# Kernel tuning notes

Measured on AMD Instinct MI355X. Metric: run time of the kernel, lower is better.

The kernel has to match this reference:

```python
import jax, jax.numpy as jnp
import numpy as np

B, S, V, E, H, DM = 4, 512, 32000, 512, 1024, 256
U, M = 4096, 1024
MEM_CAP = 512 * 4  # max_length * memory_segments


def setup_inputs() -> dict:
    key = jax.random.key(0)
    ks = jax.random.split(key, 26)
    def n(k, shape, s=0.02):
        return jax.random.normal(k, shape, dtype=jnp.float32) * s
    return {
        'input_ids': jax.random.randint(ks[0], (B, S), 0, V),
        'past_tokens': jax.random.randint(ks[1], (B, M), 0, V),
        'past_keys': jax.random.normal(ks[2], (B, M, DM), dtype=jnp.float32),
        'untied_ids': jax.random.randint(ks[3], (U,), 0, V),
        'emb': n(ks[4], (V, E)),
        'gru_w_ih': n(ks[5], (3 * H, E)), 'gru_w_hh': n(ks[6], (3 * H, H)),
        'gru_b_ih': n(ks[7], (3 * H,)), 'gru_b_hh': n(ks[8], (3 * H,)),
        'q_w': n(ks[9], (DM, H)), 'q_b': n(ks[10], (DM,)),
        'k_w': n(ks[11], (DM, H)), 'k_b': n(ks[12], (DM,)),
        'gate_w': n(ks[13], (1, H)), 'gate_b': n(ks[14], (1,)),
        'fc_w': n(ks[15], (4 * E, H)), 'fc_b': n(ks[16], (4 * E,)),
        'proj_w': n(ks[17], (E, 4 * E)), 'proj_b': n(ks[18], (E,)),
        'out_bias': jnp.zeros((V,), jnp.float32),
        'part_w': n(ks[19], (U, E)), 'part_b': n(ks[20], (U,)),
        'mem_scale': jnp.float32(6.0),
    }


def _gru(x, w_ih, w_hh, b_ih, b_hh):
    # x: [B,S,E] -> states [B,S,H]; torch GRU cell math
    xp = x @ w_ih.T + b_ih  # [B,S,3H]
    h0 = jnp.zeros((x.shape[0], w_hh.shape[1]), x.dtype)
    def step(h, xp_t):
        hp = h @ w_hh.T + b_hh
        xr, xz, xn = jnp.split(xp_t, 3, axis=-1)
        hr, hz, hn = jnp.split(hp, 3, axis=-1)
        r = jax.nn.sigmoid(xr + hr)
        z = jax.nn.sigmoid(xz + hz)
        nn_ = jnp.tanh(xn + r * hn)
        h_new = (1.0 - z) * nn_ + z * h
        return h_new, h_new
    h_last, states = jax.lax.scan(step, h0, jnp.swapaxes(xp, 0, 1))
    return jnp.swapaxes(states, 0, 1), h_last


def reference(input_ids, past_tokens, past_keys, untied_ids, emb,
              gru_w_ih, gru_w_hh, gru_b_ih, gru_b_hh,
              q_w, q_b, k_w, k_b, gate_w, gate_b,
              fc_w, fc_b, proj_w, proj_b, out_bias, part_w, part_b, mem_scale):
    x = emb[input_ids]                                  # [B,S,E]
    states, _ = _gru(x, gru_w_ih, gru_w_hh, gru_b_ih, gru_b_hh)  # dropout=eval identity
    head = jnp.square(jax.nn.relu(states @ fc_w.T + fc_b))       # [B,S,4E]
    base = head @ proj_w.T + proj_b                                # [B,S,E]
    logits = base @ emb.T + out_bias                               # [B,S,V]
    partial = base @ part_w.T + part_b                             # [B,S,U]
    logits = logits.at[:, :, untied_ids].add(partial)              # scatter_add over vocab

    q = states @ q_w.T + q_b                                       # [B,S,DM]
    ck = states @ k_w.T + k_b                                      # [B,S,DM]
    scale = jnp.float32(1.0 / np.sqrt(DM))
    cur_scores = jnp.einsum('bsd,btd->bst', q, ck) * scale
    causal = jnp.tril(jnp.ones((S, S), bool), k=-1)                # strictly-past mask
    neg = jnp.finfo(cur_scores.dtype).min
    masked_cur = jnp.where(causal[None], cur_scores, neg)
    past_scores = jnp.einsum('bsd,bmd->bsm', q, past_keys) * scale
    all_scores = jnp.concatenate([past_scores, masked_cur], axis=-1)   # [B,S,M+S]
    all_mask = jnp.concatenate([
        jnp.ones((B, S, M), bool),
        jnp.broadcast_to(causal[None], (B, S, S))], axis=-1)
    att = jax.nn.softmax(all_scores, axis=-1) * all_mask
    att = att / jnp.maximum(att.sum(axis=-1, keepdims=True), 1e-6)
    val_idx = jnp.concatenate([
        jnp.broadcast_to(past_tokens[:, None, :], (B, S, M)),
        jnp.broadcast_to(input_ids[:, None, :], (B, S, S))], axis=-1)   # [B,S,M+S]
    gate = jax.nn.sigmoid(states @ gate_w.T + gate_b)               # [B,S,1]
    gated = att * (gate * mem_scale)
    b_idx = jnp.arange(B)[:, None, None]
    s_idx = jnp.arange(S)[None, :, None]
    logits = logits.at[b_idx, s_idx, val_idx].add(gated)            # irregular scatter_add

    next_keys = jax.lax.stop_gradient(
        jnp.concatenate([past_keys, ck], axis=1))[:, -MEM_CAP:]
    next_tokens = jnp.concatenate([past_tokens, input_ids], axis=1)[:, -MEM_CAP:]
    return logits, next_keys, next_tokens
```

## Files before the change

kernel.cpp:

```cpp
#include <hip/hip_runtime.h>
#include <cstddef>
#include <cstring>

#define BB 4
#define SS 512
#define VV 32000
#define EE 512
#define HH 1024
#define DM 256
#define UU 4096
#define MM 1024
#define TT 1536

typedef __attribute__((ext_vector_type(8))) short short8v;
typedef __attribute__((ext_vector_type(4))) float f32x4;

__device__ __forceinline__ unsigned long long agent_ld64(const unsigned long long* p) {
  return __hip_atomic_load(const_cast<unsigned long long*>(p), __ATOMIC_RELAXED,
                           __HIP_MEMORY_SCOPE_AGENT);
}
__device__ __forceinline__ void agent_st64(unsigned long long* p, unsigned long long v) {
  __hip_atomic_store(p, v, __ATOMIC_RELAXED, __HIP_MEMORY_SCOPE_AGENT);
}
__device__ __forceinline__ float sigmoidf_(float x) { return 1.f / (1.f + __expf(-x)); }

__device__ __forceinline__ unsigned short f2bf_rtn(float x) {
  unsigned u; __builtin_memcpy(&u, &x, 4);
  unsigned r = (u + 0x7FFFu + ((u >> 16) & 1u)) >> 16;
  return (unsigned short)r;
}
__device__ __forceinline__ float bf2f(unsigned short b) {
  unsigned u = ((unsigned)b) << 16; float f; __builtin_memcpy(&f, &u, 4); return f;
}

__global__ __launch_bounds__(256) void split_cat(
    const float* __restrict__ in, unsigned short* __restrict__ out, int n, int K)
{
  for (int i = blockIdx.x * 256 + threadIdx.x; i < n; i += gridDim.x * 256) {
    int row = i / K, col = i - row * K;
    float x = in[i];
    unsigned short h = f2bf_rtn(x);
    unsigned short l = f2bf_rtn(x - bf2f(h));
    size_t b = (size_t)row * (K << 1) + col;
    out[b] = h;
    out[b + K] = l;
  }
}

__global__ __launch_bounds__(256) void gemm_mfma_cat(
    const unsigned short* __restrict__ A2, const int* __restrict__ a_idx,
    const unsigned short* __restrict__ W2, const float* __restrict__ bias,
    float* __restrict__ C, unsigned short* __restrict__ C2,
    int K2, int N, int ldc, int act, const int* __restrict__ sidx)
{
  const int tid = threadIdx.x, lane = tid & 63, w = tid >> 6;
  const int bm = blockIdx.y * 128, bn = blockIdx.x * 128;
  const int wm = (w >> 1) * 64, wn = (w & 1) * 64;
  const int r = lane & 15, ko = (lane >> 4) * 8;

  int arow[4];
#pragma unroll
  for (int mi = 0; mi < 4; ++mi) {
    int row = bm + wm + mi * 16 + r;
    arow[mi] = a_idx ? a_idx[row] : row;
  }

  f32x4 acc[4][4] = {};

  for (int k0 = 0; k0 < K2; k0 += 32) {
    short8v a[4], b[4];
#pragma unroll
    for (int mi = 0; mi < 4; ++mi)
      a[mi] = *(const short8v*)(A2 + (size_t)arow[mi] * K2 + k0 + ko);
#pragma unroll
    for (int ni = 0; ni < 4; ++ni)
      b[ni] = *(const short8v*)(W2 + (size_t)(bn + wn + ni * 16 + r) * K2 + k0 + ko);
#pragma unroll
    for (int mi = 0; mi < 4; ++mi)
#pragma unroll
      for (int ni = 0; ni < 4; ++ni)
        acc[mi][ni] = __builtin_amdgcn_mfma_f32_16x16x32_bf16(a[mi], b[ni], acc[mi][ni], 0, 0, 0);
  }

#pragma unroll
  for (int mi = 0; mi < 4; ++mi)
#pragma unroll
    for (int ni = 0; ni < 4; ++ni) {
      const int row = bm + wm + mi * 16 + (lane >> 4) * 4;
      const int col = bn + wn + ni * 16 + (lane & 15);
      const float bv = bias[col];
#pragma unroll
      for (int i = 0; i < 4; ++i) {
        float v = acc[mi][ni][i] + bv;
        if (act == 1) { v = fmaxf(v, 0.f); v *= v; }
        if (C2) {
          unsigned short h = f2bf_rtn(v);
          unsigned short l = f2bf_rtn(v - bf2f(h));
          size_t bo = (size_t)(row + i) * (N << 1) + col;
          C2[bo] = h;
          C2[bo + N] = l;
        } else if (sidx) {
          atomicAdd(C + (size_t)(row + i) * ldc + sidx[col], v);
        } else {
          C[(size_t)(row + i) * ldc + col] = v;
        }
      }
    }
}

__global__ __launch_bounds__(256) void score_mfma_cat(
    const unsigned short* __restrict__ q2,
    const unsigned short* __restrict__ k2,
    float* __restrict__ scores)
{
  const int b = blockIdx.z;
  const unsigned short* A2 = q2 + (size_t)b * SS * (2 * DM);
  const unsigned short* W2 = k2 + (size_t)b * TT * (2 * DM);
  float* C = scores + (size_t)b * SS * TT;

  const int tid = threadIdx.x, lane = tid & 63, w = tid >> 6;
  const int bm = blockIdx.y * 128, bn = blockIdx.x * 128;
  const int wm = (w >> 1) * 64, wn = (w & 1) * 64;
  const int r = lane & 15, ko = (lane >> 4) * 8;

  f32x4 acc[4][4] = {};

  for (int k0 = 0; k0 < 2 * DM; k0 += 32) {
    short8v a[4], bfr[4];
#pragma unroll
    for (int mi = 0; mi < 4; ++mi)
      a[mi] = *(const short8v*)(A2 + (size_t)(bm + wm + mi * 16 + r) * (2 * DM) + k0 + ko);
#pragma unroll
    for (int ni = 0; ni < 4; ++ni)
      bfr[ni] = *(const short8v*)(W2 + (size_t)(bn + wn + ni * 16 + r) * (2 * DM) + k0 + ko);
#pragma unroll
    for (int mi = 0; mi < 4; ++mi)
#pragma unroll
      for (int ni = 0; ni < 4; ++ni)
        acc[mi][ni] = __builtin_amdgcn_mfma_f32_16x16x32_bf16(a[mi], bfr[ni], acc[mi][ni], 0, 0, 0);
  }

#pragma unroll
  for (int mi = 0; mi < 4; ++mi)
#pragma unroll
    for (int ni = 0; ni < 4; ++ni) {
      const int row = bm + wm + mi * 16 + (lane >> 4) * 4;
      const int col = bn + wn + ni * 16 + (lane & 15);
#pragma unroll
      for (int i = 0; i < 4; ++i)
        C[(size_t)(row + i) * TT + col] = acc[mi][ni][i];
    }
}

__global__ __launch_bounds__(256) void softmax_scatter(
    const float* __restrict__ scores,
    const float* __restrict__ ntokf,
    const float* __restrict__ gate,
    const float* __restrict__ msp,
    float* __restrict__ logits)
{
  const int lane = threadIdx.x & 63;
  const int row = (blockIdx.x << 2) + (threadIdx.x >> 6);
  const int b = row >> 9, sg = row & 511;
  const int limit = MM + sg;
  const float* sr = scores + (size_t)row * TT;

  float v[24];
  float mx = -1e30f;
#pragma unroll
  for (int i = 0; i < 24; ++i) {
    int t = (i << 6) + lane;
    v[i] = (t < limit) ? sr[t] * 0.0625f : -1e30f;
    mx = fmaxf(mx, v[i]);
  }
#pragma unroll
  for (int off = 32; off >= 1; off >>= 1) mx = fmaxf(mx, __shfl_xor(mx, off, 64));

  float sum = 0.f;
#pragma unroll
  for (int i = 0; i < 24; ++i) sum += __expf(v[i] - mx);
#pragma unroll
  for (int off = 32; off >= 1; off >>= 1) sum += __shfl_xor(sum, off, 64);

  const float fs = gate[row] * msp[0] / sum;
  const float* tokr = ntokf + b * TT;
  float* lrow = logits + (size_t)row * VV;
#pragma unroll
  for (int i = 0; i < 24; ++i) {
    int t = (i << 6) + lane;
    if (t < limit)
      atomicAdd(lrow + (int)tokr[t], __expf(v[i] - mx) * fs);
  }
}

template <int TILE, int MICRO>
__global__ __launch_bounds__(256) void gemm_k(
    const float* __restrict__ A, const int* __restrict__ a_idx,
    const float* __restrict__ W, const float* __restrict__ bias,
    float* __restrict__ C, int K, int ldc, int act, const int* __restrict__ sidx)
{
  constexpr int PITCH = TILE + 4;
  __shared__ float As[16][PITCH];
  __shared__ float Ws[16][PITCH];
  const int tid = threadIdx.x;
  const int bm = blockIdx.y * TILE, bn = blockIdx.x * TILE;
  const int tr = tid >> 4, tc = tid & 15;
  const int lk = tid & 15, lr0 = tid >> 4;
  float acc[MICRO][MICRO] = {};

  for (int k0 = 0; k0 < K; k0 += 16) {
#pragma unroll
    for (int jj = 0; jj < TILE / 16; ++jj) {
      int row = lr0 + (jj << 4);
      int am = bm + row;
      int ar = a_idx ? a_idx[am] : am;
      As[lk][row] = A[(size_t)ar * K + k0 + lk];
      Ws[lk][row] = W[(size_t)(bn + row) * K + k0 + lk];
    }
    __syncthreads();
#pragma unroll
    for (int kk = 0; kk < 16; ++kk) {
      float av[MICRO], wv[MICRO];
#pragma unroll
      for (int i = 0; i < MICRO; ++i) av[i] = As[kk][tr * MICRO + i];
#pragma unroll
      for (int j = 0; j < MICRO; ++j) wv[j] = Ws[kk][tc * MICRO + j];
#pragma unroll
      for (int i = 0; i < MICRO; ++i)
#pragma unroll
        for (int j = 0; j < MICRO; ++j) acc[i][j] += av[i] * wv[j];
    }
    __syncthreads();
  }

#pragma unroll
  for (int i = 0; i < MICRO; ++i) {
    int m = bm + tr * MICRO + i;
    float tmp[MICRO];
#pragma unroll
    for (int j = 0; j < MICRO; ++j) {
      int n = bn + tc * MICRO + j;
      float v = acc[i][j] + bias[n];
      if (act == 1) { v = fmaxf(v, 0.f); v *= v; }
      tmp[j] = v;
    }
    if (sidx) {
#pragma unroll
      for (int j = 0; j < MICRO; ++j)
        atomicAdd(C + (size_t)m * ldc + sidx[bn + tc * MICRO + j], tmp[j]);
    } else {
      float* cp = C + (size_t)m * ldc + bn + tc * MICRO;
#pragma unroll
      for (int j4 = 0; j4 < MICRO / 4; ++j4)
        *(float4*)(cp + 4 * j4) =
            make_float4(tmp[4 * j4], tmp[4 * j4 + 1], tmp[4 * j4 + 2], tmp[4 * j4 + 3]);
    }
  }
}

__global__ __launch_bounds__(512, 1) void gru_scan(
    const float* __restrict__ xp,
    const float* __restrict__ w_hh,
    const float* __restrict__ b_hh,
    float* __restrict__ states,
    unsigned long long* hbuf)
{
  __shared__ float h_lds[2][HH];
  const int tid = threadIdx.x;
  const int lane = tid & 63;
  const int wv = tid >> 6;
  const int bb = blockIdx.x >> 5;
  const int r = blockIdx.x & 31;
  const int c0 = (r << 5) + (wv << 2);

  unsigned long long* hb = hbuf + ((size_t)bb << 11);

  float wreg[4][3][16];
#pragma unroll
  for (int k = 0; k < 4; ++k)
#pragma unroll
    for (int g = 0; g < 3; ++g) {
      const float* wr = w_hh + (size_t)((g << 10) + c0 + k) * HH + lane;
#pragma unroll
      for (int i = 0; i < 16; ++i) wreg[k][g][i] = wr[i << 6];
    }
  float bh[4][3];
#pragma unroll
  for (int k = 0; k < 4; ++k)
#pragma unroll
    for (int g = 0; g < 3; ++g) bh[k][g] = b_hh[(g << 10) + c0 + k];

  for (int i = tid; i < HH; i += 512) h_lds[0][i] = 0.f;
  __syncthreads();

  for (int t = 0; t < SS; ++t) {
    const int cur = t & 1, nxt = (t + 1) & 1;
    const float* hc = h_lds[cur];

    float4 xrv, xzv, xnv, hold;
    if (lane == 0) {
      const float* xpr = xp + (size_t)((bb << 9) + t) * 3072 + c0;
      xrv = *(const float4*)(xpr);
      xzv = *(const float4*)(xpr + HH);
      xnv = *(const float4*)(xpr + 2 * HH);
      hold = *(const float4*)(hc + c0);
    }

    float acc[4][3] = {};
#pragma unroll
    for (int i = 0; i < 16; ++i) {
      float hv = hc[(i << 6) + lane];
#pragma unroll
      for (int k = 0; k < 4; ++k) {
        acc[k][0] += hv * wreg[k][0][i];
        acc[k][1] += hv * wreg[k][1][i];
        acc[k][2] += hv * wreg[k][2][i];
      }
    }
#pragma unroll
    for (int off = 32; off >= 1; off >>= 1)
#pragma unroll
      for (int k = 0; k < 4; ++k) {
        acc[k][0] += __shfl_xor(acc[k][0], off, 64);
        acc[k][1] += __shfl_xor(acc[k][1], off, 64);
        acc[k][2] += __shfl_xor(acc[k][2], off, 64);
      }

    if (lane == 0) {
      const unsigned long long tagw = ((unsigned long long)(unsigned)(t + 1)) << 32;
      float xr[4] = {xrv.x, xrv.y, xrv.z, xrv.w};
      float xz[4] = {xzv.x, xzv.y, xzv.z, xzv.w};
      float xn[4] = {xnv.x, xnv.y, xnv.z, xnv.w};
      float ho[4] = {hold.x, hold.y, hold.z, hold.w};
      float hv4[4];
#pragma unroll
      for (int k = 0; k < 4; ++k) {
        float rr = sigmoidf_(xr[k] + acc[k][0] + bh[k][0]);
        float zz = sigmoidf_(xz[k] + acc[k][1] + bh[k][1]);
        float nn = tanhf(xn[k] + rr * (acc[k][2] + bh[k][2]));
        hv4[k] = (1.f - zz) * nn + zz * ho[k];
      }
      if (t < SS - 1) {
        unsigned long long* dst = hb + ((size_t)nxt << 10) + c0;
#pragma unroll
        for (int k = 0; k < 4; ++k) {
          unsigned hbits;
          __builtin_memcpy(&hbits, &hv4[k], 4);
          agent_st64(dst + k, tagw | (unsigned long long)hbits);
        }
      }
      *(float4*)(states + (size_t)((bb << 9) + t) * HH + c0) =
          make_float4(hv4[0], hv4[1], hv4[2], hv4[3]);
    }
    if (t == SS - 1) break;

    {
      const unsigned tgt = (unsigned)(t + 1);
      const unsigned long long* src = hb + ((size_t)nxt << 10) + (tid << 1);
      unsigned long long p0, p1;
      for (;;) {
        p0 = agent_ld64(src);
        p1 = agent_ld64(src + 1);
        if ((unsigned)(p0 >> 32) >= tgt && (unsigned)(p1 >> 32) >= tgt) break;
      }
      h_lds[nxt][(tid << 1)] = __uint_as_float((unsigned)p0);
      h_lds[nxt][(tid << 1) + 1] = __uint_as_float((unsigned)p1);
    }
    __syncthreads();
  }
}

__global__ __launch_bounds__(256) void gate_kernel(
    const float* __restrict__ states, const float* __restrict__ gate_w,
    const float* __restrict__ gate_b, float* __restrict__ out)
{
  const int lane = threadIdx.x & 63;
  const int row = (blockIdx.x << 2) + (threadIdx.x >> 6);
  float s = 0.f;
#pragma unroll
  for (int i = 0; i < 16; ++i)
    s += states[(size_t)row * HH + (i << 6) + lane] * gate_w[(i << 6) + lane];
#pragma unroll
  for (int off = 32; off >= 1; off >>= 1) s += __shfl_xor(s, off, 64);
  if (lane == 0) out[row] = sigmoidf_(s + gate_b[0]);
}

__global__ __launch_bounds__(256) void copy_next(
    const float* __restrict__ past_keys, const float* __restrict__ ck,
    const int* __restrict__ past_tokens, const int* __restrict__ input_ids,
    float* __restrict__ nk, float* __restrict__ ntokf)
{
  const int i = blockIdx.x * 256 + threadIdx.x;
  if (i < BB * TT * 64) {
    int b = i / (TT * 64);
    int rem = i - b * (TT * 64);
    int t = rem >> 6, c = rem & 63;
    float4 v;
    if (t < MM) v = ((const float4*)past_keys)[((b << 10) + t) * 64 + c];
    else        v = ((const float4*)ck)[((b << 9) + (t - MM)) * 64 + c];
    ((float4*)nk)[i] = v;
  }
  if (i < BB * TT) {
    int b = i / TT, t = i - b * TT;
    int tok = (t < MM) ? past_tokens[(b << 10) + t] : input_ids[(b << 9) + t - MM];
    ntokf[i] = (float)tok;
  }
}

__global__ __launch_bounds__(256) void attn_scatter(
    const float* __restrict__ qbuf, const float* __restrict__ nk,
    const float* __restrict__ ntokf, const float* __restrict__ gate,
    const float* __restrict__ msp, float* __restrict__ logits)
{
  __shared__ float q_s[8][260];
  __shared__ float k_s[32][260];
  const int b = blockIdx.y;
  const int s0 = blockIdx.x << 3;
  const int tid = threadIdx.x, lane = tid & 63, wv = tid >> 6;
  const int half = lane >> 5, tl = lane & 31;
  const int ss = wv + (half << 2);
  const int sg = s0 + ss;
  const int limit = MM + sg;

  for (int i = tid; i < 8 * 256; i += 256)
    q_s[i >> 8][i & 255] = qbuf[(size_t)((b << 9) + s0 + (i >> 8)) * DM + (i & 255)];

  const int kr = tid >> 3, kc = (tid & 7) << 5;
  float mx = -1e30f, sum = 0.f;
  float fscale = 0.f;

  for (int pass = 0; pass < 2; ++pass) {
    if (pass == 1) {
#pragma unroll
      for (int off = 16; off >= 1; off >>= 1) {
        float mo = __shfl_xor(mx, off, 64);
        float so = __shfl_xor(sum, off, 64);
        float m2 = fmaxf(mx, mo);
        sum = sum * __expf(mx - m2) + so * __expf(mo - m2);
        mx = m2;
      }
      fscale = gate[(b << 9) + sg] * msp[0] / sum;
    }
    for (int tile = 0; tile < 48; ++tile) {
      __syncthreads();
      {
        const float4* src = (const float4*)(nk + ((size_t)(b * TT + (tile << 5) + kr) << 8) + kc);
        float4* dst = (float4*)(&k_s[kr][kc]);
#pragma unroll
        for (int u = 0; u < 8; ++u) dst[u] = src[u];
      }
      __syncthreads();
      int t = (tile << 5) + tl;
      if (t < limit) {
        float a = 0.f;
#pragma unroll 8
        for (int d = 0; d < 256; d += 4) {
          float4 kv = *(const float4*)&k_s[tl][d];
          float4 qv = *(const float4*)&q_s[ss][d];
          a += kv.x * qv.x + kv.y * qv.y + kv.z * qv.z + kv.w * qv.w;
        }
        a *= 0.0625f;
        if (pass == 0) {
          float m2 = fmaxf(mx, a);
          sum = sum * __expf(mx - m2) + __expf(a - m2);
          mx = m2;
        } else {
          int tok = (int)ntokf[b * TT + t];
          atomicAdd(logits + (size_t)((b << 9) + sg) * VV + tok,
                    __expf(a - mx) * fscale);
        }
      }
    }
  }
}

extern "C" void kernel_launch(void* const* d_in, const int* in_sizes, int n_in,
                              void* d_out, int out_size, void* d_ws, size_t ws_size,
                              hipStream_t stream) {
  (void)in_sizes; (void)n_in; (void)out_size;
  const int*   input_ids   = (const int*)  d_in[0];
  const int*   past_tokens = (const int*)  d_in[1];
  const float* past_keys   = (const float*)d_in[2];
  const int*   untied_ids  = (const int*)  d_in[3];
  const float* emb         = (const float*)d_in[4];
  const float* w_ih        = (const float*)d_in[5];
  const float* w_hh        = (const float*)d_in[6];
  const float* b_ih        = (const float*)d_in[7];
  const float* b_hh        = (const float*)d_in[8];
  const float* q_w         = (const float*)d_in[9];
  const float* q_b         = (const float*)d_in[10];
  const float* k_w         = (const float*)d_in[11];
  const float* k_b         = (const float*)d_in[12];
  const float* gate_w      = (const float*)d_in[13];
  const float* gate_b      = (const float*)d_in[14];
  const float* fc_w        = (const float*)d_in[15];
  const float* fc_b        = (const float*)d_in[16];
  const float* proj_w      = (const float*)d_in[17];
  const float* proj_b      = (const float*)d_in[18];
  const float* out_bias    = (const float*)d_in[19];
  const float* part_w      = (const float*)d_in[20];
  const float* part_b      = (const float*)d_in[21];
  const float* mem_scale   = (const float*)d_in[22];

  char* ws = (char*)d_ws;
  float* logits = (float*)d_out;
  float* nk     = logits + 65536000ll;
  float* ntokf  = logits + 67108864ll;

  const bool fast = ws_size >= 180961280ull;

  hipMemsetAsync(ws, 0, 69632, stream);

  if (fast) {
    unsigned long long* hbuf = (unsigned long long*)(ws + 4096);
    float* gatebuf = (float*)(ws + 69632);
    float* xp      = (float*)(ws + 81920);
    float* states  = (float*)(ws + 25247744);
    float* ckb     = (float*)(ws + 33636352);
    unsigned short* emb2    = (unsigned short*)(ws + 35733504);
    unsigned short* w_ih2   = (unsigned short*)(ws + 101269504);
    unsigned short* fc_w2   = (unsigned short*)(ws + 107560960);
    unsigned short* proj_w2 = (unsigned short*)(ws + 115949568);
    unsigned short* part_w2 = (unsigned short*)(ws + 120143872);
    unsigned short* q_w2    = (unsigned short*)(ws + 128532480);
    unsigned short* k_w2    = (unsigned short*)(ws + 129581056);
    unsigned short* states2 = (unsigned short*)(ws + 130629632);
    unsigned short* head2   = (unsigned short*)(ws + 139018240);
    unsigned short* base2   = (unsigned short*)(ws + 155795456);
    unsigned short* qb2     = (unsigned short*)(ws + 159989760);
    unsigned short* nk2     = (unsigned short*)(ws + 162086912);
    float* scores           = (float*)(ws + 168378368);

    split_cat<<<2048, 256, 0, stream>>>(emb, emb2, VV * EE, EE);
    split_cat<<<512, 256, 0, stream>>>(w_ih, w_ih2, 3072 * EE, EE);
    split_cat<<<512, 256, 0, stream>>>(fc_w, fc_w2, 2048 * HH, HH);
    split_cat<<<512, 256, 0, stream>>>(proj_w, proj_w2, EE * 2048, 2048);
    split_cat<<<512, 256, 0, stream>>>(part_w, part_w2, UU * EE, EE);
    split_cat<<<128, 256, 0, stream>>>(q_w, q_w2, DM * HH, HH);
    split_cat<<<128, 256, 0, stream>>>(k_w, k_w2, DM * HH, HH);

    gemm_mfma_cat<<<dim3(3072 / 128, 2048 / 128), 256, 0, stream>>>(
        emb2, input_ids, w_ih2, b_ih, xp, nullptr, 2 * EE, 3072, 3072, 0, nullptr);

    gru_scan<<<128, 512, 0, stream>>>(xp, w_hh, b_hh, states, hbuf);
    split_cat<<<512, 256, 0, stream>>>(states, states2, 2048 * HH, HH);

    gemm_mfma_cat<<<dim3(2048 / 128, 2048 / 128), 256, 0, stream>>>(
        states2, nullptr, fc_w2, fc_b, nullptr, head2, 2 * HH, 2048, 0, 1, nullptr);

    gemm_mfma_cat<<<dim3(512 / 128, 2048 / 128), 256, 0, stream>>>(
        head2, nullptr, proj_w2, proj_b, nullptr, base2, 2 * 2048, EE, 0, 0, nullptr);

    gemm_mfma_cat<<<dim3(VV / 128, 2048 / 128), 256, 0, stream>>>(
        base2, nullptr, emb2, out_bias, logits, nullptr, 2 * EE, VV, VV, 0, nullptr);

    gemm_mfma_cat<<<dim3(UU / 128, 2048 / 128), 256, 0, stream>>>(
        base2, nullptr, part_w2, part_b, logits, nullptr, 2 * EE, UU, VV, 0, untied_ids);

    gemm_mfma_cat<<<dim3(DM / 128, 2048 / 128), 256, 0, stream>>>(
        states2, nullptr, q_w2, q_b, nullptr, qb2, 2 * HH, DM, 0, 0, nullptr);
    gemm_mfma_cat<<<dim3(DM / 128, 2048 / 128), 256, 0, stream>>>(
        states2, nullptr, k_w2, k_b, ckb, nullptr, 2 * HH, DM, DM, 0, nullptr);

    gate_kernel<<<512, 256, 0, stream>>>(states, gate_w, gate_b, gatebuf);

    copy_next<<<1536, 256, 0, stream>>>(past_keys, ckb, past_tokens, input_ids, nk, ntokf);

    split_cat<<<512, 256, 0, stream>>>(nk, nk2, BB * TT * DM, DM);
    score_mfma_cat<<<dim3(TT / 128, SS / 128, BB), 256, 0, stream>>>(qb2, nk2, scores);
    softmax_scatter<<<512, 256, 0, stream>>>(scores, ntokf, gatebuf, mem_scale, logits);
  } else {
    unsigned long long* hbuf = (unsigned long long*)(ws + 4096);
    float* gatebuf  = (float*)(ws + 69632);
    float* qb       = (float*)(ws + 81920);
    float* ckb      = (float*)(ws + 2179072);
    float* xp       = (float*)(ws + 4276224);
    float* states   = (float*)(ws + 29442048);
    float* head     = (float*)(ws + 37830656);
    float* base     = (float*)(ws + 54607872);

    gemm_k<128, 8><<<dim3(3072 / 128, 2048 / 128), 256, 0, stream>>>(
        emb, input_ids, w_ih, b_ih, xp, EE, 3072, 0, nullptr);
    gru_scan<<<128, 512, 0, stream>>>(xp, w_hh, b_hh, states, hbuf);
    gemm_k<128, 8><<<dim3(2048 / 128, 2048 / 128), 256, 0, stream>>>(
        states, nullptr, fc_w, fc_b, head, HH, 2048, 1, nullptr);
    gemm_k<64, 4><<<dim3(512 / 64, 2048 / 64), 256, 0, stream>>>(
        head, nullptr, proj_w, proj_b, base, 2048, EE, 0, nullptr);
    gemm_k<128, 8><<<dim3(VV / 128, 2048 / 128), 256, 0, stream>>>(
        base, nullptr, emb, out_bias, logits, EE, VV, 0, nullptr);
    gemm_k<128, 8><<<dim3(UU / 128, 2048 / 128), 256, 0, stream>>>(
        base, nullptr, part_w, part_b, logits, EE, VV, 0, untied_ids);
    gemm_k<64, 4><<<dim3(DM / 64, 2048 / 64), 256, 0, stream>>>(
        states, nullptr, q_w, q_b, qb, HH, DM, 0, nullptr);
    gemm_k<64, 4><<<dim3(DM / 64, 2048 / 64), 256, 0, stream>>>(
        states, nullptr, k_w, k_b, ckb, HH, DM, 0, nullptr);
    gate_kernel<<<512, 256, 0, stream>>>(states, gate_w, gate_b, gatebuf);
    copy_next<<<1536, 256, 0, stream>>>(past_keys, ckb, past_tokens, input_ids, nk, ntokf);
    attn_scatter<<<dim3(SS / 8, BB), 256, 0, stream>>>(qb, nk, ntokf, gatebuf, mem_scale, logits);
  }
}
```

Before: 4.937 ms.

## Overlap weight bf16 splitting with GRU scan using extra idle blocks

The GRU scan kernel is launched with 64 extra blocks that perform the hi/lo bf16 splitting of the emb, fc, proj, part, q and k weights while the 128 scan blocks run the serial recurrence. The input projection now gathers and splits only the 2048 embedding rows it needs instead of waiting on the full vocabulary split. This moves the split work onto CUs left idle during the latency-bound scan. The risk is that the extra blocks compete for memory bandwidth and could slow the scan's cross-block synchronisation. If the scan relies on all its blocks being co-resident, the larger grid also has to fit on the device at once. The workspace requirement grows to hold the gathered rows.

New measurement: 4.998 ms. Within noise of the previous version (+1.2%).

```diff
diff --git a/kernel.cpp b/kernel.cpp
--- a/kernel.cpp
+++ b/kernel.cpp
@@ -33,6 +33,22 @@
   unsigned u = ((unsigned)b) << 16; float f; __builtin_memcpy(&f, &u, 4); return f;
 }
 
+__device__ __forceinline__ void split_range(
+    const float* __restrict__ in, unsigned short* __restrict__ out,
+    int n, int K, int sw, int nsw, int tid)
+{
+  for (size_t i = (size_t)sw * 512 + tid; i < (size_t)n; i += (size_t)nsw * 512) {
+    int row = (int)(i / (size_t)K);
+    int col = (int)(i - (size_t)row * K);
+    float x = in[i];
+    unsigned short h = f2bf_rtn(x);
+    unsigned short l = f2bf_rtn(x - bf2f(h));
+    size_t b = (size_t)row * ((size_t)K << 1) + col;
+    out[b] = h;
+    out[b + K] = l;
+  }
+}
+
 __global__ __launch_bounds__(256) void split_cat(
     const float* __restrict__ in, unsigned short* __restrict__ out, int n, int K)
 {
@@ -44,6 +60,21 @@
     size_t b = (size_t)row * (K << 1) + col;
     out[b] = h;
     out[b + K] = l;
+  }
+}
+
+__global__ __launch_bounds__(256) void gather_split_rows(
+    const float* __restrict__ emb, const int* __restrict__ ids,
+    unsigned short* __restrict__ out)
+{
+  int i = blockIdx.x * 256 + threadIdx.x;
+  if (i < 2048 * EE) {
+    int row = i >> 9, col = i & 511;
+    float x = emb[(size_t)ids[row] * EE + col];
+    unsigned short h = f2bf_rtn(x);
+    unsigned short l = f2bf_rtn(x - bf2f(h));
+    out[(size_t)row * (2 * EE) + col] = h;
+    out[(size_t)row * (2 * EE) + col + EE] = l;
   }
 }
 
@@ -263,10 +294,29 @@
     const float* __restrict__ w_hh,
     const float* __restrict__ b_hh,
     float* __restrict__ states,
-    unsigned long long* hbuf)
+    unsigned long long* hbuf,
+    const float* __restrict__ embp,  unsigned short* emb2p,
+    const float* __restrict__ fcp,   unsigned short* fc2p,
+    const float* __restrict__ projp, unsigned short* proj2p,
+    const float* __restrict__ partp, unsigned short* part2p,
+    const float* __restrict__ qp,    unsigned short* q2p,
+    const float* __restrict__ kp,    unsigned short* k2p)
 {
   __shared__ float h_lds[2][HH];
   const int tid = threadIdx.x;
+
+  if (blockIdx.x >= 128) {
+    const int sw = blockIdx.x - 128;
+    const int nsw = gridDim.x - 128;
+    split_range(embp,  emb2p,  VV * EE,   EE,   sw, nsw, tid);
+    split_range(fcp,   fc2p,   2048 * HH, HH,   sw, nsw, tid);
+    split_range(projp, proj2p, EE * 2048, 2048, sw, nsw, tid);
+    split_range(partp, part2p, UU * EE,   EE,   sw, nsw, tid);
+    split_range(qp,    q2p,    DM * HH,   HH,   sw, nsw, tid);
+    split_range(kp,    k2p,    DM * HH,   HH,   sw, nsw, tid);
+    return;
+  }
+
   const int lane = tid & 63;
   const int wv = tid >> 6;
   const int bb = blockIdx.x >> 5;
@@ -507,7 +557,7 @@
   float* nk     = logits + 65536000ll;
   float* ntokf  = logits + 67108864ll;
 
-  const bool fast = ws_size >= 180961280ull;
+  const bool fast = ws_size >= 185155584ull;
 
   hipMemsetAsync(ws, 0, 69632, stream);
 
@@ -530,19 +580,17 @@
     unsigned short* qb2     = (unsigned short*)(ws + 159989760);
     unsigned short* nk2     = (unsigned short*)(ws + 162086912);
     float* scores           = (float*)(ws + 168378368);
-
-    split_cat<<<2048, 256, 0, stream>>>(emb, emb2, VV * EE, EE);
+    unsigned short* embrows2 = (unsigned short*)(ws + 180961280);
+
     split_cat<<<512, 256, 0, stream>>>(w_ih, w_ih2, 3072 * EE, EE);
-    split_cat<<<512, 256, 0, stream>>>(fc_w, fc_w2, 2048 * HH, HH);
-    split_cat<<<512, 256, 0, stream>>>(proj_w, proj_w2, EE * 2048, 2048);
-    split_cat<<<512, 256, 0, stream>>>(part_w, part_w2, UU * EE, EE);
-    split_cat<<<128, 256, 0, stream>>>(q_w, q_w2, DM * HH, HH);
-    split_cat<<<128, 256, 0, stream>>>(k_w, k_w2, DM * HH, HH);
+    gather_split_rows<<<4096, 256, 0, stream>>>(emb, input_ids, embrows2);
 
     gemm_mfma_cat<<<dim3(3072 / 128, 2048 / 128), 256, 0, stream>>>(
-        emb2, input_ids, w_ih2, b_ih, xp, nullptr, 2 * EE, 3072, 3072, 0, nullptr);
-
-    gru_scan<<<128, 512, 0, stream>>>(xp, w_hh, b_hh, states, hbuf);
+        embrows2, nullptr, w_ih2, b_ih, xp, nullptr, 2 * EE, 3072, 3072, 0, nullptr);
+
+    gru_scan<<<192, 512, 0, stream>>>(xp, w_hh, b_hh, states, hbuf,
+                                      emb, emb2, fc_w, fc_w2, proj_w, proj_w2,
+                                      part_w, part_w2, q_w, q_w2, k_w, k_w2);
     split_cat<<<512, 256, 0, stream>>>(states, states2, 2048 * HH, HH);
 
     gemm_mfma_cat<<<dim3(2048 / 128, 2048 / 128), 256, 0, stream>>>(
@@ -581,7 +629,9 @@
 
     gemm_k<128, 8><<<dim3(3072 / 128, 2048 / 128), 256, 0, stream>>>(
         emb, input_ids, w_ih, b_ih, xp, EE, 3072, 0, nullptr);
-    gru_scan<<<128, 512, 0, stream>>>(xp, w_hh, b_hh, states, hbuf);
+    gru_scan<<<128, 512, 0, stream>>>(xp, w_hh, b_hh, states, hbuf,
+                                      nullptr, nullptr, nullptr, nullptr, nullptr, nullptr,
+                                      nullptr, nullptr, nullptr, nullptr, nullptr, nullptr);
     gemm_k<128, 8><<<dim3(2048 / 128, 2048 / 128), 256, 0, stream>>>(
         states, nullptr, fc_w, fc_b, head, HH, 2048, 1, nullptr);
     gemm_k<64, 4><<<dim3(512 / 64, 2048 / 64), 256, 0, stream>>>(
```
